# Kernel optimization log

Hardware: AMD Instinct MI355X
Metric: run time of the kernel (lower is better)

The kernel has to match this reference:

```python
import jax, jax.numpy as jnp
import numpy as np

B, T, U = 8, 200, 100
D_ENC = D_DEC = J = 512
V = 1024


def setup_inputs() -> dict:
    key = jax.random.key(0)
    ks = jax.random.split(key, 7)
    s = 0.02
    return {
        "enc_out": jax.random.normal(ks[0], (B, T, 1, D_ENC), jnp.float32),
        "dec_out": jax.random.normal(ks[1], (B, 1, U, D_DEC), jnp.float32),
        "W_enc": jax.random.normal(ks[2], (J, D_ENC), jnp.float32) * s,
        "b_enc": jax.random.normal(ks[3], (J,), jnp.float32) * s,
        "W_dec": jax.random.normal(ks[4], (J, D_DEC), jnp.float32) * s,
        "W_out": jax.random.normal(ks[5], (V, J), jnp.float32) * s,
        "b_out": jax.random.normal(ks[6], (V,), jnp.float32) * s,
    }


def reference(enc_out, dec_out, W_enc, b_enc, W_dec, W_out, b_out):
    # lin_enc: (B,T,1,J); lin_dec (no bias): (B,1,U,J)
    enc_proj = jnp.einsum('btod,jd->btoj', enc_out, W_enc) + b_enc
    dec_proj = jnp.einsum('boud,jd->bouj', dec_out, W_dec)
    # broadcast add -> (B,T,U,J), tanh activation
    joint = jnp.tanh(enc_proj + dec_proj)
    # lin_out -> (B,T,U,V)
    return jnp.einsum('btuj,vj->btuv', joint, W_out) + b_out
```

## Files before the change

kernel.cpp:

```cpp
#include <hip/hip_runtime.h>


#define B_ 8
#define T_ 200
#define U_ 100
#define J_ 512
#define V_ 1024
#define M2_ (B_ * T_ * U_)

typedef __attribute__((ext_vector_type(4))) float float4v;
typedef __attribute__((ext_vector_type(8))) short short8;
typedef __attribute__((ext_vector_type(4))) float f32x4;

#define DEV static __device__ __forceinline__

DEV unsigned short f2bf(float f) {
  unsigned int u = __float_as_uint(f);
  u += 0x7FFFu + ((u >> 16) & 1u);
  return (unsigned short)(u >> 16);
}

DEV short8 pack8(float4v a, float4v b) {
  short8 r;
  r[0] = (short)f2bf(a[0]); r[1] = (short)f2bf(a[1]);
  r[2] = (short)f2bf(a[2]); r[3] = (short)f2bf(a[3]);
  r[4] = (short)f2bf(b[0]); r[5] = (short)f2bf(b[1]);
  r[6] = (short)f2bf(b[2]); r[7] = (short)f2bf(b[3]);
  return r;
}

DEV float fast_tanh(float x) {
  float t = __expf(2.0f * x);
  float r = __builtin_amdgcn_rcpf(t + 1.0f);
  return __builtin_fmaf(-2.0f, r, 1.0f);
}

#define SWZ(base, row, kb) ((base) + ((row) << 7) + ((((kb) ^ ((row) & 7))) << 4))

__global__ __launch_bounds__(256) void convert_wout(
    const float* __restrict__ W, unsigned short* __restrict__ Wb) {
  int i = blockIdx.x * 256 + threadIdx.x;
  const float* p = W + (size_t)i * 8;
  float4v a = *(const float4v*)p;
  float4v b = *(const float4v*)(p + 4);
  *(short8*)(Wb + (size_t)i * 8) = pack8(a, b);
}

__global__ __launch_bounds__(256) void proj_kernel(
    const float* __restrict__ enc_out, const float* __restrict__ dec_out,
    const float* __restrict__ W_enc, const float* __restrict__ b_enc,
    const float* __restrict__ W_dec,
    float* __restrict__ enc_proj, float* __restrict__ dec_proj) {
  __shared__ char lds[16384];
  char* Albs = lds;
  char* Blbs = lds + 8192;

  int bid = blockIdx.x;
  bool is_enc = bid < 200;
  const float* srcA;
  const float* Wsrc;
  float* dst;
  int Mrows, bm, bn;
  if (is_enc) {
    bm = bid >> 3; bn = bid & 7;
    srcA = enc_out; Wsrc = W_enc; dst = enc_proj; Mrows = 1600;
  } else {
    int q = bid - 200;
    bm = q >> 3; bn = q & 7;
    srcA = dec_out; Wsrc = W_dec; dst = dec_proj; Mrows = 800;
  }

  int t = threadIdx.x;
  int l = t & 63;
  int w = t >> 6;
  int wrow = w >> 1, wcol = w & 1;

  f32x4 acc[2][2] = {};

  for (int k0 = 0; k0 < 512; k0 += 64) {
#pragma unroll
    for (int i = 0; i < 2; ++i) {
      int g = t + i * 256;
      int row = g >> 3, kb = g & 7;
      int arow = bm * 64 + row;
      if (arow >= Mrows) arow = Mrows - 1;
      const float* pa = srcA + (size_t)arow * 512 + k0 + kb * 8;
      *(short8*)SWZ(Albs, row, kb) =
          pack8(*(const float4v*)pa, *(const float4v*)(pa + 4));
      const float* pb = Wsrc + (size_t)(bn * 64 + row) * 512 + k0 + kb * 8;
      *(short8*)SWZ(Blbs, row, kb) =
          pack8(*(const float4v*)pb, *(const float4v*)(pb + 4));
    }
    __syncthreads();
#pragma unroll
    for (int h = 0; h < 2; ++h) {
      int kb = h * 4 + (l >> 4);
      short8 af[2], bfv[2];
#pragma unroll
      for (int m = 0; m < 2; ++m) {
        int row = wrow * 32 + m * 16 + (l & 15);
        af[m] = *(const short8*)SWZ(Albs, row, kb);
      }
#pragma unroll
      for (int n = 0; n < 2; ++n) {
        int row = wcol * 32 + n * 16 + (l & 15);
        bfv[n] = *(const short8*)SWZ(Blbs, row, kb);
      }
#pragma unroll
      for (int m = 0; m < 2; ++m)
#pragma unroll
        for (int n = 0; n < 2; ++n)
          acc[m][n] = __builtin_amdgcn_mfma_f32_16x16x32_bf16(
              af[m], bfv[n], acc[m][n], 0, 0, 0);
    }
    __syncthreads();
  }

#pragma unroll
  for (int n = 0; n < 2; ++n) {
    int col = bn * 64 + wcol * 32 + n * 16 + (l & 15);
    float bias = is_enc ? b_enc[col] : 0.0f;
#pragma unroll
    for (int m = 0; m < 2; ++m) {
#pragma unroll
      for (int j = 0; j < 4; ++j) {
        int gr = bm * 64 + wrow * 32 + m * 16 + (l >> 4) * 4 + j;
        if (gr < Mrows) dst[(size_t)gr * 512 + col] = acc[m][n][j] + bias;
      }
    }
  }
}

__global__ __launch_bounds__(256) void joint_kernel(
    const float* __restrict__ enc_proj, const float* __restrict__ dec_proj,
    const unsigned short* __restrict__ Wb, const float* __restrict__ b_out,
    float* __restrict__ out) {
  __shared__ char lds[32768];
  char* Albs = lds;
  char* Blbs = lds + 16384;

  int bid = blockIdx.x;
  int bm = bid >> 3;
  int bn = bid & 7;

  int t = threadIdx.x;
  int l = t & 63;
  int w = t >> 6;
  int wrow = w >> 1, wcol = w & 1;

  int erow[4], drow[4];
  int kbA = t & 7;
#pragma unroll
  for (int i = 0; i < 4; ++i) {
    int row = (t >> 3) + i * 32;
    int gr = bm * 128 + row;
    int b_ = gr / 20000;
    int rem = gr - b_ * 20000;
    int u_ = rem % 100;
    erow[i] = gr / 100;
    drow[i] = b_ * 100 + u_;
  }

  f32x4 acc[4][4] = {};

  for (int k0 = 0; k0 < 512; k0 += 64) {
#pragma unroll
    for (int i = 0; i < 4; ++i) {
      int g = t + i * 256;
      int row = g >> 3;
      int kbp = g & 7;
      int kb = kbp ^ (row & 7);
      const unsigned short* src =
          Wb + (size_t)(bn * 128 + row) * 512 + k0 + kb * 8;
      __builtin_amdgcn_global_load_lds(
          (const __attribute__((address_space(1))) unsigned int*)src,
          (__attribute__((address_space(3))) unsigned int*)(Blbs + (w * 64 + i * 256) * 16),
          16, 0, 0);
    }
#pragma unroll
    for (int i = 0; i < 4; ++i) {
      int row = (t >> 3) + i * 32;
      const float* pe = enc_proj + (size_t)erow[i] * 512 + k0 + kbA * 8;
      const float* pd = dec_proj + (size_t)drow[i] * 512 + k0 + kbA * 8;
      float4v e0 = *(const float4v*)pe;
      float4v e1 = *(const float4v*)(pe + 4);
      float4v d0 = *(const float4v*)pd;
      float4v d1 = *(const float4v*)(pd + 4);
      float4v j0, j1;
#pragma unroll
      for (int q = 0; q < 4; ++q) {
        j0[q] = fast_tanh(e0[q] + d0[q]);
        j1[q] = fast_tanh(e1[q] + d1[q]);
      }
      *(short8*)SWZ(Albs, row, kbA) = pack8(j0, j1);
    }
    __syncthreads();

#pragma unroll
    for (int h = 0; h < 2; ++h) {
      int kb = h * 4 + (l >> 4);
      short8 af[4], bfv[4];
#pragma unroll
      for (int m = 0; m < 4; ++m) {
        int row = wrow * 64 + m * 16 + (l & 15);
        af[m] = *(const short8*)SWZ(Albs, row, kb);
      }
#pragma unroll
      for (int n = 0; n < 4; ++n) {
        int row = wcol * 64 + n * 16 + (l & 15);
        bfv[n] = *(const short8*)SWZ(Blbs, row, kb);
      }
#pragma unroll
      for (int m = 0; m < 4; ++m)
#pragma unroll
        for (int n = 0; n < 4; ++n)
          acc[m][n] = __builtin_amdgcn_mfma_f32_16x16x32_bf16(
              af[m], bfv[n], acc[m][n], 0, 0, 0);
    }
    __syncthreads();
  }

  int colbase = bn * 128 + wcol * 64;
#pragma unroll
  for (int n = 0; n < 4; ++n) {
    int col = colbase + n * 16 + (l & 15);
    float bias = b_out[col];
#pragma unroll
    for (int m = 0; m < 4; ++m) {
      int grb = bm * 128 + wrow * 64 + m * 16 + (l >> 4) * 4;
#pragma unroll
      for (int j = 0; j < 4; ++j) {
        out[(size_t)(grb + j) * 1024 + col] = acc[m][n][j] + bias;
      }
    }
  }
}

extern "C" void kernel_launch(void* const* d_in, const int* in_sizes, int n_in,
                              void* d_out, int out_size, void* d_ws, size_t ws_size,
                              hipStream_t stream) {
  const float* enc_out = (const float*)d_in[0];
  const float* dec_out = (const float*)d_in[1];
  const float* W_enc   = (const float*)d_in[2];
  const float* b_enc   = (const float*)d_in[3];
  const float* W_dec   = (const float*)d_in[4];
  const float* W_out   = (const float*)d_in[5];
  const float* b_out   = (const float*)d_in[6];
  float* out = (float*)d_out;

  char* ws = (char*)d_ws;
  float* enc_proj = (float*)ws;
  float* dec_proj = (float*)(ws + 3276800);
  unsigned short* Wb = (unsigned short*)(ws + 3276800 + 1638400);

  hipLaunchKernelGGL(convert_wout, dim3(256), dim3(256), 0, stream, W_out, Wb);
  hipLaunchKernelGGL(proj_kernel, dim3(304), dim3(256), 0, stream,
                     enc_out, dec_out, W_enc, b_enc, W_dec, enc_proj, dec_proj);
  hipLaunchKernelGGL(joint_kernel, dim3((M2_ / 128) * 8), dim3(256), 0, stream,
                     enc_proj, dec_proj, Wb, b_out, out);
}
```

Measured before the change: 963.7 us.

## Compute tanh joint strip once per row block and stream W_out tiles

The joint kernel now has each 512-thread block compute a full 128x512 bf16 tanh(enc+dec) strip into LDS once, then loop over all eight 128-column W_out tiles with double-buffered async global-to-LDS loads and MFMA priority hints. This removes the eightfold recomputation of tanh and reloading of enc/dec projections that the old per-(bm,bn) grid performed. The cost is 160KB of LDS per block, so only one block fits per CU and occupancy drops. The grid also shrinks to 1250 blocks, and the output stores are now interleaved with compute.

```diff
diff --git a/kernel.cpp b/kernel.cpp
--- a/kernel.cpp
+++ b/kernel.cpp
@@ -35,8 +35,6 @@
   return __builtin_fmaf(-2.0f, r, 1.0f);
 }
 
-#define SWZ(base, row, kb) ((base) + ((row) << 7) + ((((kb) ^ ((row) & 7))) << 4))
-
 __global__ __launch_bounds__(256) void convert_wout(
     const float* __restrict__ W, unsigned short* __restrict__ Wb) {
   int i = blockIdx.x * 256 + threadIdx.x;
@@ -45,6 +43,8 @@
   float4v b = *(const float4v*)(p + 4);
   *(short8*)(Wb + (size_t)i * 8) = pack8(a, b);
 }
+
+#define SWZ64(base, row, kb) ((base) + ((row) << 7) + ((((kb) ^ ((row) & 7))) << 4))
 
 __global__ __launch_bounds__(256) void proj_kernel(
     const float* __restrict__ enc_out, const float* __restrict__ dec_out,
@@ -85,10 +85,10 @@
       int arow = bm * 64 + row;
       if (arow >= Mrows) arow = Mrows - 1;
       const float* pa = srcA + (size_t)arow * 512 + k0 + kb * 8;
-      *(short8*)SWZ(Albs, row, kb) =
+      *(short8*)SWZ64(Albs, row, kb) =
           pack8(*(const float4v*)pa, *(const float4v*)(pa + 4));
       const float* pb = Wsrc + (size_t)(bn * 64 + row) * 512 + k0 + kb * 8;
-      *(short8*)SWZ(Blbs, row, kb) =
+      *(short8*)SWZ64(Blbs, row, kb) =
           pack8(*(const float4v*)pb, *(const float4v*)(pb + 4));
     }
     __syncthreads();
@@ -99,12 +99,12 @@
 #pragma unroll
       for (int m = 0; m < 2; ++m) {
         int row = wrow * 32 + m * 16 + (l & 15);
-        af[m] = *(const short8*)SWZ(Albs, row, kb);
+        af[m] = *(const short8*)SWZ64(Albs, row, kb);
       }
 #pragma unroll
       for (int n = 0; n < 2; ++n) {
         int row = wcol * 32 + n * 16 + (l & 15);
-        bfv[n] = *(const short8*)SWZ(Blbs, row, kb);
+        bfv[n] = *(const short8*)SWZ64(Blbs, row, kb);
       }
 #pragma unroll
       for (int m = 0; m < 2; ++m)
@@ -131,57 +131,54 @@
   }
 }
 
-__global__ __launch_bounds__(256) void joint_kernel(
+__global__ __launch_bounds__(512) void joint_kernel(
     const float* __restrict__ enc_proj, const float* __restrict__ dec_proj,
     const unsigned short* __restrict__ Wb, const float* __restrict__ b_out,
     float* __restrict__ out) {
-  __shared__ char lds[32768];
-  char* Albs = lds;
-  char* Blbs = lds + 16384;
-
-  int bid = blockIdx.x;
-  int bm = bid >> 3;
-  int bn = bid & 7;
-
+  __shared__ char lds[163840];
+  char* Astrip = lds;
+  char* Bbuf0 = lds + 131072;
+  char* Bbuf1 = lds + 131072 + 16384;
+
+  int bm = blockIdx.x;
   int t = threadIdx.x;
   int l = t & 63;
   int w = t >> 6;
-  int wrow = w >> 1, wcol = w & 1;
-
-  int erow[4], drow[4];
-  int kbA = t & 7;
-#pragma unroll
-  for (int i = 0; i < 4; ++i) {
-    int row = (t >> 3) + i * 32;
+  int wrow = w >> 2;
+  int wcol = w & 3;
+
+  {
+#pragma unroll
+    for (int i = 0; i < 2; ++i) {
+      int g = t + i * 512;
+      int rowc = g >> 3;
+      int kbp = g & 7;
+      int kb = kbp ^ (rowc & 7);
+      const unsigned short* src = Wb + (size_t)rowc * 512 + kb * 8;
+      __builtin_amdgcn_global_load_lds(
+          (const __attribute__((address_space(1))) unsigned int*)src,
+          (__attribute__((address_space(3))) unsigned int*)(Bbuf0 + g * 16),
+          16, 0, 0);
+    }
+  }
+
+  {
+    int row = t >> 2;
     int gr = bm * 128 + row;
     int b_ = gr / 20000;
     int rem = gr - b_ * 20000;
     int u_ = rem % 100;
-    erow[i] = gr / 100;
-    drow[i] = b_ * 100 + u_;
-  }
-
-  f32x4 acc[4][4] = {};
-
-  for (int k0 = 0; k0 < 512; k0 += 64) {
-#pragma unroll
-    for (int i = 0; i < 4; ++i) {
-      int g = t + i * 256;
-      int row = g >> 3;
-      int kbp = g & 7;
-      int kb = kbp ^ (row & 7);
-      const unsigned short* src =
-          Wb + (size_t)(bn * 128 + row) * 512 + k0 + kb * 8;
-      __builtin_amdgcn_global_load_lds(
-          (const __attribute__((address_space(1))) unsigned int*)src,
-          (__attribute__((address_space(3))) unsigned int*)(Blbs + (w * 64 + i * 256) * 16),
-          16, 0, 0);
-    }
-#pragma unroll
-    for (int i = 0; i < 4; ++i) {
-      int row = (t >> 3) + i * 32;
-      const float* pe = enc_proj + (size_t)erow[i] * 512 + k0 + kbA * 8;
-      const float* pd = dec_proj + (size_t)drow[i] * 512 + k0 + kbA * 8;
+    int erow = gr / 100;
+    int drow = b_ * 100 + u_;
+    const float* pe_base = enc_proj + (size_t)erow * 512;
+    const float* pd_base = dec_proj + (size_t)drow * 512;
+    char* arow_base = Astrip + row * 1024;
+    int swz = row & 7;
+#pragma unroll
+    for (int i = 0; i < 16; ++i) {
+      int kb = i * 4 + (t & 3);
+      const float* pe = pe_base + kb * 8;
+      const float* pd = pd_base + kb * 8;
       float4v e0 = *(const float4v*)pe;
       float4v e1 = *(const float4v*)(pe + 4);
       float4v d0 = *(const float4v*)pd;
@@ -192,47 +189,84 @@
         j0[q] = fast_tanh(e0[q] + d0[q]);
         j1[q] = fast_tanh(e1[q] + d1[q]);
       }
-      *(short8*)SWZ(Albs, row, kbA) = pack8(j0, j1);
-    }
-    __syncthreads();
-
-#pragma unroll
-    for (int h = 0; h < 2; ++h) {
-      int kb = h * 4 + (l >> 4);
-      short8 af[4], bfv[4];
+      *(short8*)(arow_base + ((kb ^ swz) << 4)) = pack8(j0, j1);
+    }
+  }
+  __syncthreads();
+
+  f32x4 acc[4][2] = {{{0.f,0.f,0.f,0.f}}};
+#pragma unroll
+  for (int m = 0; m < 4; ++m)
+#pragma unroll
+    for (int n = 0; n < 2; ++n)
+      acc[m][n] = (f32x4){0.f, 0.f, 0.f, 0.f};
+
+  for (int s = 0; s < 64; ++s) {
+    char* Bcur = (s & 1) ? Bbuf1 : Bbuf0;
+    char* Bnxt = (s & 1) ? Bbuf0 : Bbuf1;
+
+    if (s < 63) {
+      int nt1 = (s + 1) >> 3;
+      int k01 = ((s + 1) & 7) * 64;
+#pragma unroll
+      for (int i = 0; i < 2; ++i) {
+        int g = t + i * 512;
+        int rowc = g >> 3;
+        int kbp = g & 7;
+        int kb = kbp ^ (rowc & 7);
+        const unsigned short* src =
+            Wb + (size_t)(nt1 * 128 + rowc) * 512 + k01 + kb * 8;
+        __builtin_amdgcn_global_load_lds(
+            (const __attribute__((address_space(1))) unsigned int*)src,
+            (__attribute__((address_space(3))) unsigned int*)(Bnxt + g * 16),
+            16, 0, 0);
+      }
+    }
+
+    int k0g = (s & 7) * 8;
+#pragma unroll
+    for (int kk = 0; kk < 2; ++kk) {
+      short8 af[4], bfv[2];
+      int kbA = k0g + kk * 4 + (l >> 4);
 #pragma unroll
       for (int m = 0; m < 4; ++m) {
-        int row = wrow * 64 + m * 16 + (l & 15);
-        af[m] = *(const short8*)SWZ(Albs, row, kb);
-      }
-#pragma unroll
-      for (int n = 0; n < 4; ++n) {
-        int row = wcol * 64 + n * 16 + (l & 15);
-        bfv[n] = *(const short8*)SWZ(Blbs, row, kb);
-      }
+        int r = wrow * 64 + m * 16 + (l & 15);
+        af[m] = *(const short8*)(Astrip + r * 1024 + (((kbA ^ (r & 7))) << 4));
+      }
+      int kbB = kk * 4 + (l >> 4);
+#pragma unroll
+      for (int n = 0; n < 2; ++n) {
+        int rc = wcol * 32 + n * 16 + (l & 15);
+        bfv[n] = *(const short8*)(Bcur + rc * 128 + (((kbB ^ (rc & 7))) << 4));
+      }
+      __builtin_amdgcn_s_setprio(1);
 #pragma unroll
       for (int m = 0; m < 4; ++m)
 #pragma unroll
-        for (int n = 0; n < 4; ++n)
+        for (int n = 0; n < 2; ++n)
           acc[m][n] = __builtin_amdgcn_mfma_f32_16x16x32_bf16(
               af[m], bfv[n], acc[m][n], 0, 0, 0);
-    }
+      __builtin_amdgcn_s_setprio(0);
+    }
+
+    if ((s & 7) == 7) {
+      int nt = s >> 3;
+#pragma unroll
+      for (int n = 0; n < 2; ++n) {
+        int col = nt * 128 + wcol * 32 + n * 16 + (l & 15);
+        float bias = b_out[col];
+#pragma unroll
+        for (int m = 0; m < 4; ++m) {
+          int r0 = bm * 128 + wrow * 64 + m * 16 + (l >> 4) * 4;
+#pragma unroll
+          for (int j = 0; j < 4; ++j)
+            out[(size_t)(r0 + j) * 1024 + col] = acc[m][n][j] + bias;
+          acc[m][n] = (f32x4){0.f, 0.f, 0.f, 0.f};
+        }
+      }
+    }
+
     __syncthreads();
-  }
-
-  int colbase = bn * 128 + wcol * 64;
-#pragma unroll
-  for (int n = 0; n < 4; ++n) {
-    int col = colbase + n * 16 + (l & 15);
-    float bias = b_out[col];
-#pragma unroll
-    for (int m = 0; m < 4; ++m) {
-      int grb = bm * 128 + wrow * 64 + m * 16 + (l >> 4) * 4;
-#pragma unroll
-      for (int j = 0; j < 4; ++j) {
-        out[(size_t)(grb + j) * 1024 + col] = acc[m][n][j] + bias;
-      }
-    }
   }
 }
 
@@ -256,6 +290,6 @@
   hipLaunchKernelGGL(convert_wout, dim3(256), dim3(256), 0, stream, W_out, Wb);
   hipLaunchKernelGGL(proj_kernel, dim3(304), dim3(256), 0, stream,
                      enc_out, dec_out, W_enc, b_enc, W_dec, enc_proj, dec_proj);
-  hipLaunchKernelGGL(joint_kernel, dim3((M2_ / 128) * 8), dim3(256), 0, stream,
+  hipLaunchKernelGGL(joint_kernel, dim3(M2_ / 128), dim3(512), 0, stream,
                      enc_proj, dec_proj, Wb, b_out, out);
 }
```

After: 856.7 us. -11.1%, faster.
